# Kernel optimization log

Hardware: AMD Instinct MI355X
Metric: run time of the kernel (lower is better)

## Reference

```python
import jax, jax.numpy as jnp
import numpy as np

B, N, D, H, F = 2, 2048, 1024, 16, 4096
E = D // H
EPS = 1e-5

def layer_norm(x, g, b):
    mu = jnp.mean(x, axis=-1, keepdims=True)
    var = jnp.var(x, axis=-1, keepdims=True)
    return (x - mu) * jax.lax.rsqrt(var + EPS) * g + b

def setup_inputs() -> dict:
    key = jax.random.key(0)
    ks = jax.random.split(key, 16)
    s = lambda k, sh, fan: jax.random.normal(k, sh, jnp.float32) * (1.0 / np.sqrt(fan))
    return {
        'x': jax.random.normal(ks[0], (B, N, D), jnp.float32),
        'wq': s(ks[1], (D, D), D), 'bq': jnp.zeros((D,), jnp.float32),
        'wk': s(ks[2], (D, D), D), 'bk': jnp.zeros((D,), jnp.float32),
        'wv': s(ks[3], (D, D), D), 'bv': jnp.zeros((D,), jnp.float32),
        'w1': s(ks[4], (F, D), D), 'b1': jnp.zeros((F,), jnp.float32),
        'ln_mlp_g': jnp.ones((F,), jnp.float32), 'ln_mlp_b': jnp.zeros((F,), jnp.float32),
        'w2': s(ks[5], (D, F), F), 'b2': jnp.zeros((D,), jnp.float32),
        'ln1_g': jnp.ones((D,), jnp.float32), 'ln1_b': jnp.zeros((D,), jnp.float32),
        'ln2_g': jnp.ones((D,), jnp.float32), 'ln2_b': jnp.zeros((D,), jnp.float32),
    }

def reference(x, wq, bq, wk, bk, wv, bv, w1, b1, ln_mlp_g, ln_mlp_b, w2, b2, ln1_g, ln1_b, ln2_g, ln2_b):
    h = layer_norm(x, ln1_g, ln1_b)                       # [B,N,D]
    q = (h @ wq.T + bq).reshape(B, N, H, E).transpose(0, 2, 1, 3)  # [B,H,N,E]
    k = (h @ wk.T + bk).reshape(B, N, H, E).transpose(0, 2, 1, 3)
    v = (h @ wv.T + bv).reshape(B, N, H, E).transpose(0, 2, 1, 3)
    # faithful to source: score = q@k^T / sqrt(1/emb_dim) == q@k^T * sqrt(emb_dim)
    score = jnp.einsum('bhne,bhme->bhnm', q, k) * np.sqrt(D).astype(np.float32)
    causal = jnp.tril(jnp.ones((N, N), bool))
    score = jnp.where(causal[None, None], score, -jnp.inf)
    weight = jax.nn.softmax(score, axis=-1)
    attn = jnp.einsum('bhnm,bhme->bhne', weight, v)       # [B,H,N,E]
    attn = attn.transpose(0, 2, 1, 3).reshape(B, N, D)
    x = x + attn
    h2 = layer_norm(x, ln2_g, ln2_b)
    m = h2 @ w1.T + b1                                    # [B,N,F]
    m = jax.nn.relu(layer_norm(m, ln_mlp_g, ln_mlp_b))
    # faithful: no second residual in the source forward
    return m @ w2.T + b2
```

## Files before the change

### kernel.cpp

```cpp
#include <hip/hip_runtime.h>
#include <cstdint>

typedef __bf16 bf16_t;
typedef bf16_t bf16x8 __attribute__((ext_vector_type(8)));
typedef bf16_t bf16x4 __attribute__((ext_vector_type(4)));
typedef float  floatx4 __attribute__((ext_vector_type(4)));

#define GLD_LDS(g, l) __builtin_amdgcn_global_load_lds( \
    (const __attribute__((address_space(1))) unsigned int*)(g), \
    (__attribute__((address_space(3))) unsigned int*)(l), 16, 0, 0)

#define MFMA_BF16_16x16x32 __builtin_amdgcn_mfma_f32_16x16x32_bf16

__global__ __launch_bounds__(256) void prep(
    const float* __restrict__ wq, const float* __restrict__ wk,
    const float* __restrict__ wv, const float* __restrict__ w1,
    const float* __restrict__ w2, const float* __restrict__ bq,
    const float* __restrict__ bk,
    bf16_t* __restrict__ wqk_hi, bf16_t* __restrict__ wqk_lo,
    bf16_t* __restrict__ wvb, bf16_t* __restrict__ w1b, bf16_t* __restrict__ w2b,
    float* __restrict__ bqk) {
  const int blk = blockIdx.x, tid = threadIdx.x;
  if (blk < 2048) {
    const int qk = blk >> 10;
    const int i  = (blk & 1023) * 256 + tid;
    const float* src = qk ? wk : wq;
    float4 v = ((const float4*)src)[i];
    float f[4] = {v.x, v.y, v.z, v.w};
    bf16x4 h, l;
    #pragma unroll
    for (int j = 0; j < 4; ++j) { h[j] = (bf16_t)f[j]; l[j] = (bf16_t)(f[j] - (float)h[j]); }
    ((bf16x4*)(wqk_hi + qk * 1024 * 1024))[i] = h;
    ((bf16x4*)(wqk_lo + qk * 1024 * 1024))[i] = l;
  } else if (blk < 3072) {
    const int i = (blk - 2048) * 256 + tid;
    float4 v = ((const float4*)wv)[i];
    bf16x4 o; o[0]=(bf16_t)v.x; o[1]=(bf16_t)v.y; o[2]=(bf16_t)v.z; o[3]=(bf16_t)v.w;
    ((bf16x4*)wvb)[i] = o;
  } else if (blk < 7168) {
    const int i = (blk - 3072) * 256 + tid;
    float4 v = ((const float4*)w1)[i];
    bf16x4 o; o[0]=(bf16_t)v.x; o[1]=(bf16_t)v.y; o[2]=(bf16_t)v.z; o[3]=(bf16_t)v.w;
    ((bf16x4*)w1b)[i] = o;
  } else if (blk < 11264) {
    const int i = (blk - 7168) * 256 + tid;
    float4 v = ((const float4*)w2)[i];
    bf16x4 o; o[0]=(bf16_t)v.x; o[1]=(bf16_t)v.y; o[2]=(bf16_t)v.z; o[3]=(bf16_t)v.w;
    ((bf16x4*)w2b)[i] = o;
  } else {
    const int i = (blk - 11264) * 256 + tid;
    if (i < 1024) { bqk[i] = bq[i]; bqk[1024 + i] = bk[i]; }
  }
}


__device__ __forceinline__ void block_sum2(float& s, float& ss, float* red) {
  #pragma unroll
  for (int off = 32; off > 0; off >>= 1) {
    s  += __shfl_down(s, off);
    ss += __shfl_down(ss, off);
  }
  const int wave = threadIdx.x >> 6;
  if ((threadIdx.x & 63) == 0) { red[wave * 2] = s; red[wave * 2 + 1] = ss; }
  __syncthreads();
  s  = red[0] + red[2] + red[4] + red[6];
  ss = red[1] + red[3] + red[5] + red[7];
}

__global__ __launch_bounds__(256) void ln_fwd_split(const float* __restrict__ x,
    const float* __restrict__ g, const float* __restrict__ b,
    bf16_t* __restrict__ out_hi, bf16_t* __restrict__ out_lo) {
  __shared__ float red[8];
  const size_t row = blockIdx.x;
  float4 v = ((const float4*)(x + row * 1024))[threadIdx.x];
  float s  = v.x + v.y + v.z + v.w;
  float ss = v.x*v.x + v.y*v.y + v.z*v.z + v.w*v.w;
  block_sum2(s, ss, red);
  const float mu  = s * (1.f / 1024.f);
  const float var = ss * (1.f / 1024.f) - mu * mu;
  const float rs  = rsqrtf(var + 1e-5f);
  float4 gg = ((const float4*)g)[threadIdx.x];
  float4 bb = ((const float4*)b)[threadIdx.x];
  float f[4];
  f[0] = (v.x - mu) * rs * gg.x + bb.x;
  f[1] = (v.y - mu) * rs * gg.y + bb.y;
  f[2] = (v.z - mu) * rs * gg.z + bb.z;
  f[3] = (v.w - mu) * rs * gg.w + bb.w;
  bf16x4 oh, ol;
  #pragma unroll
  for (int j = 0; j < 4; ++j) {
    oh[j] = (bf16_t)f[j];
    ol[j] = (bf16_t)(f[j] - (float)oh[j]);
  }
  ((bf16x4*)(out_hi + row * 1024))[threadIdx.x] = oh;
  ((bf16x4*)(out_lo + row * 1024))[threadIdx.x] = ol;
}

__global__ __launch_bounds__(256) void resid_ln_fwd(const float* __restrict__ x,
    const float* __restrict__ a, const float* __restrict__ g, const float* __restrict__ b,
    bf16_t* __restrict__ out) {
  __shared__ float red[8];
  const size_t row = blockIdx.x;
  float4 v = ((const float4*)(x + row * 1024))[threadIdx.x];
  float4 av = ((const float4*)(a + row * 1024))[threadIdx.x];
  v.x += av.x; v.y += av.y; v.z += av.z; v.w += av.w;
  float s  = v.x + v.y + v.z + v.w;
  float ss = v.x*v.x + v.y*v.y + v.z*v.z + v.w*v.w;
  block_sum2(s, ss, red);
  const float mu  = s * (1.f / 1024.f);
  const float var = ss * (1.f / 1024.f) - mu * mu;
  const float rs  = rsqrtf(var + 1e-5f);
  float4 gg = ((const float4*)g)[threadIdx.x];
  float4 bb = ((const float4*)b)[threadIdx.x];
  bf16x4 o;
  o[0] = (bf16_t)((v.x - mu) * rs * gg.x + bb.x);
  o[1] = (bf16_t)((v.y - mu) * rs * gg.y + bb.y);
  o[2] = (bf16_t)((v.z - mu) * rs * gg.z + bb.z);
  o[3] = (bf16_t)((v.w - mu) * rs * gg.w + bb.w);
  ((bf16x4*)(out + row * 1024))[threadIdx.x] = o;
}

__global__ __launch_bounds__(256) void ln_relu_inplace(bf16_t* __restrict__ m,
    const float* __restrict__ g, const float* __restrict__ b) {
  __shared__ float red[8];
  const size_t row = blockIdx.x;
  bf16_t* mr = m + row * 4096;
  const int base = threadIdx.x * 16;
  bf16x8 v0 = *(bf16x8*)(mr + base);
  bf16x8 v1 = *(bf16x8*)(mr + base + 8);
  float f[16];
  #pragma unroll
  for (int i = 0; i < 8; ++i) { f[i] = (float)v0[i]; f[8 + i] = (float)v1[i]; }
  float s = 0.f, ss = 0.f;
  #pragma unroll
  for (int i = 0; i < 16; ++i) { s += f[i]; ss += f[i] * f[i]; }
  block_sum2(s, ss, red);
  const float mu  = s * (1.f / 4096.f);
  const float var = ss * (1.f / 4096.f) - mu * mu;
  const float rs  = rsqrtf(var + 1e-5f);
  bf16x8 o0, o1;
  #pragma unroll
  for (int i = 0; i < 16; ++i) {
    float ov = (f[i] - mu) * rs * g[base + i] + b[base + i];
    ov = fmaxf(ov, 0.f);
    if (i < 8) o0[i] = (bf16_t)ov; else o1[i - 8] = (bf16_t)ov;
  }
  *(bf16x8*)(mr + base) = o0;
  *(bf16x8*)(mr + base + 8) = o1;
}

template <int OUT_MODE, int BM>
__global__ __launch_bounds__(256) void gemm_bt(
    const bf16_t* __restrict__ A, const bf16_t* __restrict__ Bw,
    const float* __restrict__ bias, void* __restrict__ Cp,
    int M, int N, int K) {
  constexpr int MI = BM / 32;
  __shared__ bf16_t As[BM * 32];
  __shared__ bf16_t Bs[128 * 32];
  const int tid  = threadIdx.x;
  const int wave = tid >> 6, lane = tid & 63;
  const int quad = lane >> 4, l15 = lane & 15;
  const int m0 = blockIdx.x * BM, n0 = blockIdx.y * 128;
  const int wm = (wave >> 1) * (BM / 2), wn = (wave & 1) * 64;
  const int srowA = wave * (BM / 4) + (lane >> 2);
  const int srowB = wave * 32 + (lane >> 2);
  const int scol = (lane & 3) * 8;

  floatx4 acc[MI][4] = {};

  const bf16_t* Ag = A  + (size_t)(m0 + srowA) * K + scol;
  const bf16_t* Bg = Bw + (size_t)(n0 + srowB) * K + scol;

  for (int k0 = 0; k0 < K; k0 += 32) {
    __syncthreads();
    #pragma unroll
    for (int i = 0; i < BM / 64; ++i)
      GLD_LDS(Ag + (size_t)(i * 16) * K + k0, As + wave * (BM / 4) * 32 + i * 512);
    #pragma unroll
    for (int i = 0; i < 2; ++i)
      GLD_LDS(Bg + (size_t)(i * 16) * K + k0, Bs + wave * 1024 + i * 512);
    __syncthreads();
    bf16x8 af[MI], bfr[4];
    #pragma unroll
    for (int i = 0; i < MI; ++i)
      af[i] = *(const bf16x8*)(As + (wm + i * 16 + l15) * 32 + quad * 8);
    #pragma unroll
    for (int j = 0; j < 4; ++j)
      bfr[j] = *(const bf16x8*)(Bs + (wn + j * 16 + l15) * 32 + quad * 8);
    #pragma unroll
    for (int i = 0; i < MI; ++i)
      #pragma unroll
      for (int j = 0; j < 4; ++j)
        acc[i][j] = MFMA_BF16_16x16x32(af[i], bfr[j], acc[i][j], 0, 0, 0);
  }
  #pragma unroll
  for (int j = 0; j < 4; ++j) {
    const int col = n0 + wn + j * 16 + l15;
    const float bv = bias[col];
    #pragma unroll
    for (int i = 0; i < MI; ++i) {
      #pragma unroll
      for (int r = 0; r < 4; ++r) {
        const int row = m0 + wm + i * 16 + quad * 4 + r;
        const float v = acc[i][j][r] + bv;
        if (OUT_MODE == 0) {
          ((float*)Cp)[(size_t)row * N + col] = v;
        } else if (OUT_MODE == 1) {
          ((bf16_t*)Cp)[(size_t)row * N + col] = (bf16_t)v;
        } else {
          const int b = row >> 11, n = row & 2047;
          const int h = col >> 6, e = col & 63;
          ((bf16_t*)Cp)[(((size_t)((b << 4) + h) * 2048 + n) << 6) + e] = (bf16_t)v;
        }
      }
    }
  }
}

__global__ __launch_bounds__(256) void gemm_qk_split(
    const bf16_t* __restrict__ Ah, const bf16_t* __restrict__ Al,
    const bf16_t* __restrict__ Bh, const bf16_t* __restrict__ Bl,
    const float* __restrict__ bias,
    bf16_t* __restrict__ qhi, bf16_t* __restrict__ qlo,
    bf16_t* __restrict__ khi, bf16_t* __restrict__ klo,
    int M, int N, int K) {
  __shared__ bf16_t Ash[64 * 32];
  __shared__ bf16_t Asl[64 * 32];
  __shared__ bf16_t Bsh[128 * 32];
  __shared__ bf16_t Bsl[128 * 32];
  const int tid  = threadIdx.x;
  const int wave = tid >> 6, lane = tid & 63;
  const int quad = lane >> 4, l15 = lane & 15;
  const int m0 = blockIdx.x * 64, n0 = blockIdx.y * 128;
  const int wm = (wave >> 1) * 32, wn = (wave & 1) * 64;
  const int srowA = wave * 16 + (lane >> 2);
  const int srowB = wave * 32 + (lane >> 2);
  const int scol = (lane & 3) * 8;

  floatx4 acc[2][4] = {};

  const size_t aoff = (size_t)(m0 + srowA) * K + scol;
  const size_t boff = (size_t)(n0 + srowB) * K + scol;

  for (int k0 = 0; k0 < K; k0 += 32) {
    __syncthreads();
    GLD_LDS(Ah + aoff + k0, Ash + wave * 512);
    GLD_LDS(Al + aoff + k0, Asl + wave * 512);
    #pragma unroll
    for (int i = 0; i < 2; ++i) {
      const size_t gb = boff + (size_t)(i * 16) * K + k0;
      GLD_LDS(Bh + gb, Bsh + wave * 1024 + i * 512);
      GLD_LDS(Bl + gb, Bsl + wave * 1024 + i * 512);
    }
    __syncthreads();
    bf16x8 ah[2], al[2], bh[4], bl[4];
    #pragma unroll
    for (int i = 0; i < 2; ++i) {
      const int ro = (wm + i * 16 + l15) * 32 + quad * 8;
      ah[i] = *(const bf16x8*)(Ash + ro);
      al[i] = *(const bf16x8*)(Asl + ro);
    }
    #pragma unroll
    for (int j = 0; j < 4; ++j) {
      const int ro = (wn + j * 16 + l15) * 32 + quad * 8;
      bh[j] = *(const bf16x8*)(Bsh + ro);
      bl[j] = *(const bf16x8*)(Bsl + ro);
    }
    #pragma unroll
    for (int i = 0; i < 2; ++i)
      #pragma unroll
      for (int j = 0; j < 4; ++j) {
        acc[i][j] = MFMA_BF16_16x16x32(ah[i], bh[j], acc[i][j], 0, 0, 0);
        acc[i][j] = MFMA_BF16_16x16x32(ah[i], bl[j], acc[i][j], 0, 0, 0);
        acc[i][j] = MFMA_BF16_16x16x32(al[i], bh[j], acc[i][j], 0, 0, 0);
      }
  }
  #pragma unroll
  for (int j = 0; j < 4; ++j) {
    const int col = n0 + wn + j * 16 + l15;
    const float bv = bias[col];
    const bool isq = col < 1024;
    bf16_t* hib = isq ? qhi : khi;
    bf16_t* lob = isq ? qlo : klo;
    const float scale = isq ? 32.0f : 1.0f;
    const int h = (col >> 6) & 15, e = col & 63;
    #pragma unroll
    for (int i = 0; i < 2; ++i) {
      #pragma unroll
      for (int r = 0; r < 4; ++r) {
        const int row = m0 + wm + i * 16 + quad * 4 + r;
        const int b = row >> 11, n = row & 2047;
        const float c = (acc[i][j][r] + bv) * scale;
        const bf16_t chi = (bf16_t)c;
        const bf16_t clo = (bf16_t)(c - (float)chi);
        const size_t dst = (((size_t)((b << 4) + h) * 2048 + n) << 6) + e;
        hib[dst] = chi;
        lob[dst] = clo;
      }
    }
  }
}

__global__ __launch_bounds__(256) void transpose_v(
    const bf16_t* __restrict__ vhm, bf16_t* __restrict__ vT) {
  __shared__ bf16_t T[64 * 72];
  const int bh = blockIdx.x, n0 = blockIdx.y * 64;
  const int r = threadIdx.x >> 2;
  const int c = (threadIdx.x & 3) * 16;
  const bf16_t* src = vhm + ((size_t)bh * 2048 + n0 + r) * 64 + c;
  bf16x8 a0 = *(const bf16x8*)src;
  bf16x8 a1 = *(const bf16x8*)(src + 8);
  #pragma unroll
  for (int j = 0; j < 8; ++j) {
    T[(c + j) * 72 + r]     = a0[j];
    T[(c + 8 + j) * 72 + r] = a1[j];
  }
  __syncthreads();
  bf16x8 o0 = *(const bf16x8*)(T + r * 72 + c);
  bf16x8 o1 = *(const bf16x8*)(T + r * 72 + c + 8);
  bf16_t* dst = vT + ((size_t)(bh * 64 + r)) * 2048 + n0 + c;
  *(bf16x8*)dst = o0;
  *(bf16x8*)(dst + 8) = o1;
}

__global__ __launch_bounds__(256, 4) void attn_causal(
    const bf16_t* __restrict__ qhi, const bf16_t* __restrict__ qlo,
    const bf16_t* __restrict__ khi, const bf16_t* __restrict__ klo,
    const bf16_t* __restrict__ vT, float* __restrict__ o) {
  __shared__ bf16_t KsH[64 * 72];
  __shared__ bf16_t KsL[64 * 72];
  __shared__ bf16_t Vt[64 * 72];
  __shared__ bf16_t Ps[4][16 * 70];

  const int tid  = threadIdx.x;
  const int wave = tid >> 6, lane = tid & 63;
  const int quad = lane >> 4, l15 = lane & 15;
  const int bh = blockIdx.x;
  const int q0 = (31 - (int)blockIdx.y) * 64;
  const size_t hb = (size_t)bh * 2048;

  const int wmin = q0 + wave * 16;
  bf16x8 qh[2], ql[2];
  {
    const bf16_t* qbh = qhi + ((hb + wmin + l15) << 6) + quad * 8;
    const bf16_t* qbl = qlo + ((hb + wmin + l15) << 6) + quad * 8;
    qh[0] = *(const bf16x8*)qbh;
    qh[1] = *(const bf16x8*)(qbh + 32);
    ql[0] = *(const bf16x8*)qbl;
    ql[1] = *(const bf16x8*)(qbl + 32);
  }

  floatx4 accO[4] = {};
  float m_row[4] = {-1e30f, -1e30f, -1e30f, -1e30f};
  float l_row[4] = {};

  const int kr = wave * 16 + (lane >> 3);
  const int kc = (lane & 7) * 8;
  const bf16_t* kgh = khi + ((hb + kr) << 6) + kc;
  const bf16_t* kgl = klo + ((hb + kr) << 6) + kc;
  const bf16_t* vg  = vT + ((size_t)(bh * 64 + kr)) * 2048 + kc;

  bf16x8 pkh0 = *(const bf16x8*)(kgh);
  bf16x8 pkh1 = *(const bf16x8*)(kgh + (8 << 6));
  bf16x8 pkl0 = *(const bf16x8*)(kgl);
  bf16x8 pkl1 = *(const bf16x8*)(kgl + (8 << 6));
  bf16x8 pv0  = *(const bf16x8*)(vg);
  bf16x8 pv1  = *(const bf16x8*)(vg + 8 * 2048);

  const int ntiles = (q0 >> 6) + 1;
  for (int t = 0; t < ntiles; ++t) {
    const int k0 = t * 64;
    __syncthreads();
    *(bf16x8*)(KsH + kr * 72 + kc)       = pkh0;
    *(bf16x8*)(KsH + (kr + 8) * 72 + kc) = pkh1;
    *(bf16x8*)(KsL + kr * 72 + kc)       = pkl0;
    *(bf16x8*)(KsL + (kr + 8) * 72 + kc) = pkl1;
    *(bf16x8*)(Vt  + kr * 72 + kc)       = pv0;
    *(bf16x8*)(Vt  + (kr + 8) * 72 + kc) = pv1;
    if (t + 1 < ntiles) {
      const int koff = (t + 1) << 12;
      pkh0 = *(const bf16x8*)(kgh + koff);
      pkh1 = *(const bf16x8*)(kgh + koff + (8 << 6));
      pkl0 = *(const bf16x8*)(kgl + koff);
      pkl1 = *(const bf16x8*)(kgl + koff + (8 << 6));
      pv0  = *(const bf16x8*)(vg + (t + 1) * 64);
      pv1  = *(const bf16x8*)(vg + (t + 1) * 64 + 8 * 2048);
    }
    __syncthreads();

    const bool needmask = (k0 + 63 > wmin);

    floatx4 sv[4];
    #pragma unroll
    for (int j = 0; j < 4; ++j) {
      const bf16_t* kbh = KsH + (j * 16 + l15) * 72;
      const bf16_t* kbl = KsL + (j * 16 + l15) * 72;
      const bf16x8 kh0 = *(const bf16x8*)(kbh + quad * 8);
      const bf16x8 kh1 = *(const bf16x8*)(kbh + 32 + quad * 8);
      const bf16x8 kl0 = *(const bf16x8*)(kbl + quad * 8);
      const bf16x8 kl1 = *(const bf16x8*)(kbl + 32 + quad * 8);
      floatx4 acc = {};
      acc = MFMA_BF16_16x16x32(qh[0], kh0, acc, 0, 0, 0);
      acc = MFMA_BF16_16x16x32(qh[1], kh1, acc, 0, 0, 0);
      acc = MFMA_BF16_16x16x32(qh[0], kl0, acc, 0, 0, 0);
      acc = MFMA_BF16_16x16x32(qh[1], kl1, acc, 0, 0, 0);
      acc = MFMA_BF16_16x16x32(ql[0], kh0, acc, 0, 0, 0);
      acc = MFMA_BF16_16x16x32(ql[1], kh1, acc, 0, 0, 0);
      sv[j] = acc;
    }

    const int colb = k0 + l15;
    #pragma unroll
    for (int r = 0; r < 4; ++r) {
      const int rowg = wmin + quad * 4 + r;
      float sr[4], mr = -1e30f;
      #pragma unroll
      for (int j = 0; j < 4; ++j) {
        float x = sv[j][r];
        if (needmask && (colb + j * 16 > rowg)) x = -1e30f;
        sr[j] = x;
        mr = fmaxf(mr, x);
      }
      mr = fmaxf(mr, __shfl_xor(mr, 1));
      mr = fmaxf(mr, __shfl_xor(mr, 2));
      mr = fmaxf(mr, __shfl_xor(mr, 4));
      mr = fmaxf(mr, __shfl_xor(mr, 8));
      const float mnew = fmaxf(m_row[r], mr);
      const float alpha = __expf(m_row[r] - mnew);
      m_row[r] = mnew;
      float psum = 0.f;
      #pragma unroll
      for (int j = 0; j < 4; ++j) {
        const float p = __expf(sr[j] - mnew);
        const bf16_t pb = (bf16_t)p;
        psum += (float)pb;
        Ps[wave][(quad * 4 + r) * 70 + j * 16 + l15] = pb;
      }
      psum += __shfl_xor(psum, 1);
      psum += __shfl_xor(psum, 2);
      psum += __shfl_xor(psum, 4);
      psum += __shfl_xor(psum, 8);
      l_row[r] = l_row[r] * alpha + psum;
      #pragma unroll
      for (int j = 0; j < 4; ++j) accO[j][r] *= alpha;
    }
    asm volatile("s_waitcnt lgkmcnt(0)" ::: "memory");

    bf16x8 pf[2];
    {
      const bf16_t* pr = &Ps[wave][l15 * 70];
      pf[0] = *(const bf16x8*)(pr + quad * 8);
      pf[1] = *(const bf16x8*)(pr + 32 + quad * 8);
    }
    #pragma unroll
    for (int j = 0; j < 4; ++j) {
      const bf16_t* vb = Vt + (j * 16 + l15) * 72;
      const bf16x8 vf0 = *(const bf16x8*)(vb + quad * 8);
      const bf16x8 vf1 = *(const bf16x8*)(vb + 32 + quad * 8);
      accO[j] = MFMA_BF16_16x16x32(pf[0], vf0, accO[j], 0, 0, 0);
      accO[j] = MFMA_BF16_16x16x32(pf[1], vf1, accO[j], 0, 0, 0);
    }
  }

  const int b = bh >> 4, h = bh & 15;
  #pragma unroll
  for (int r = 0; r < 4; ++r) {
    const float linv = 1.f / l_row[r];
    const int qr = wmin + quad * 4 + r;
    float* orow = o + ((size_t)(b * 2048) + qr) * 1024 + h * 64;
    #pragma unroll
    for (int j = 0; j < 4; ++j)
      orow[j * 16 + l15] = accO[j][r] * linv;
  }
}


extern "C" void kernel_launch(void* const* d_in, const int* in_sizes, int n_in,
                              void* d_out, int out_size, void* d_ws, size_t ws_size,
                              hipStream_t stream) {
  const float* x        = (const float*)d_in[0];
  const float* wq       = (const float*)d_in[1];
  const float* bq       = (const float*)d_in[2];
  const float* wk       = (const float*)d_in[3];
  const float* bk       = (const float*)d_in[4];
  const float* wv       = (const float*)d_in[5];
  const float* bv       = (const float*)d_in[6];
  const float* w1       = (const float*)d_in[7];
  const float* b1       = (const float*)d_in[8];
  const float* ln_mlp_g = (const float*)d_in[9];
  const float* ln_mlp_b = (const float*)d_in[10];
  const float* w2       = (const float*)d_in[11];
  const float* b2       = (const float*)d_in[12];
  const float* ln1_g    = (const float*)d_in[13];
  const float* ln1_b    = (const float*)d_in[14];
  const float* ln2_g    = (const float*)d_in[15];
  const float* ln2_b    = (const float*)d_in[16];

  char* ws = (char*)d_ws;
  bf16_t* h_hi   = (bf16_t*)(ws);
  bf16_t* h_lo   = (bf16_t*)(ws + (8u  << 20));
  bf16_t* vTb    = (bf16_t*)(ws);
  bf16_t* wqk_hi = (bf16_t*)(ws + (16u << 20));
  bf16_t* wqk_lo = (bf16_t*)(ws + (20u << 20));
  bf16_t* wvb    = (bf16_t*)(ws + (24u << 20));
  float*  bqk    = (float*) (ws + (26u << 20));
  bf16_t* w1b    = (bf16_t*)(ws + (28u << 20));
  bf16_t* w2b    = (bf16_t*)(ws + (36u << 20));
  bf16_t* qhi    = (bf16_t*)(ws + (44u << 20));
  bf16_t* qlo    = (bf16_t*)(ws + (52u << 20));
  bf16_t* khi    = (bf16_t*)(ws + (60u << 20));
  bf16_t* klo    = (bf16_t*)(ws + (68u << 20));
  bf16_t* mbuf   = (bf16_t*)(ws + (44u << 20));
  bf16_t* vhm    = (bf16_t*)(ws + (76u << 20));
  float*  attnb  = (float*) (ws + (84u << 20));
  bf16_t* h2     = (bf16_t*)(ws + (100u << 20));

  prep<<<11268, 256, 0, stream>>>(wq, wk, wv, w1, w2, bq, bk,
                                  wqk_hi, wqk_lo, wvb, w1b, w2b, bqk);

  ln_fwd_split<<<4096, 256, 0, stream>>>(x, ln1_g, ln1_b, h_hi, h_lo);
  gemm_qk_split<<<dim3(64, 16), 256, 0, stream>>>(h_hi, h_lo, wqk_hi, wqk_lo, bqk,
                                                  qhi, qlo, khi, klo, 4096, 2048, 1024);
  gemm_bt<2, 64><<<dim3(64, 8), 256, 0, stream>>>(h_hi, wvb, bv, vhm, 4096, 1024, 1024);
  transpose_v<<<dim3(32, 32), 256, 0, stream>>>(vhm, vTb);
  attn_causal<<<dim3(32, 32), 256, 0, stream>>>(qhi, qlo, khi, klo, vTb, attnb);
  resid_ln_fwd<<<4096, 256, 0, stream>>>(x, attnb, ln2_g, ln2_b, h2);
  gemm_bt<1, 128><<<dim3(32, 32), 256, 0, stream>>>(h2, w1b, b1, mbuf, 4096, 4096, 1024);
  ln_relu_inplace<<<4096, 256, 0, stream>>>(mbuf, ln_mlp_g, ln_mlp_b);
  gemm_bt<0, 64><<<dim3(64, 8), 256, 0, stream>>>(mbuf, w2b, b2, d_out, 4096, 1024, 4096);

  (void)in_sizes; (void)n_in; (void)out_size; (void)ws_size;
}
```

Baseline: 478.0 us.

## Transpose QK^T MFMA so each lane owns one query row in softmax

Swaps the MFMA operand order so the score tile comes out transposed, giving each lane a single query row across 16 key columns. Row max and sum then need only two cross-lane shuffles instead of four per row times four rows, and the running m/l statistics shrink to one scalar per lane. P is written to LDS as bf16x4 vectors rather than scalar stores. The accumulator rescale is skipped when no row max changed in the wave. In exchange it adds shuffles to broadcast alpha and l back to the output layout.

After: 472.8 us. Within noise of the previous version (-1.1%).

```diff
diff --git a/kernel.cpp b/kernel.cpp
--- a/kernel.cpp
+++ b/kernel.cpp
@@ -340,6 +340,7 @@
   const size_t hb = (size_t)bh * 2048;
 
   const int wmin = q0 + wave * 16;
+  const int qrow = wmin + l15;
   bf16x8 qh[2], ql[2];
   {
     const bf16_t* qbh = qhi + ((hb + wmin + l15) << 6) + quad * 8;
@@ -351,8 +352,8 @@
   }
 
   floatx4 accO[4] = {};
-  float m_row[4] = {-1e30f, -1e30f, -1e30f, -1e30f};
-  float l_row[4] = {};
+  float m_row = -1e30f;
+  float l_row = 0.f;
 
   const int kr = wave * 16 + (lane >> 3);
   const int kc = (lane & 7) * 8;
@@ -400,49 +401,59 @@
       const bf16x8 kl0 = *(const bf16x8*)(kbl + quad * 8);
       const bf16x8 kl1 = *(const bf16x8*)(kbl + 32 + quad * 8);
       floatx4 acc = {};
-      acc = MFMA_BF16_16x16x32(qh[0], kh0, acc, 0, 0, 0);
-      acc = MFMA_BF16_16x16x32(qh[1], kh1, acc, 0, 0, 0);
-      acc = MFMA_BF16_16x16x32(qh[0], kl0, acc, 0, 0, 0);
-      acc = MFMA_BF16_16x16x32(qh[1], kl1, acc, 0, 0, 0);
-      acc = MFMA_BF16_16x16x32(ql[0], kh0, acc, 0, 0, 0);
-      acc = MFMA_BF16_16x16x32(ql[1], kh1, acc, 0, 0, 0);
+      acc = MFMA_BF16_16x16x32(kh0, qh[0], acc, 0, 0, 0);
+      acc = MFMA_BF16_16x16x32(kh1, qh[1], acc, 0, 0, 0);
+      acc = MFMA_BF16_16x16x32(kl0, qh[0], acc, 0, 0, 0);
+      acc = MFMA_BF16_16x16x32(kl1, qh[1], acc, 0, 0, 0);
+      acc = MFMA_BF16_16x16x32(kh0, ql[0], acc, 0, 0, 0);
+      acc = MFMA_BF16_16x16x32(kh1, ql[1], acc, 0, 0, 0);
       sv[j] = acc;
     }
 
-    const int colb = k0 + l15;
-    #pragma unroll
-    for (int r = 0; r < 4; ++r) {
-      const int rowg = wmin + quad * 4 + r;
-      float sr[4], mr = -1e30f;
-      #pragma unroll
-      for (int j = 0; j < 4; ++j) {
+    const int lim = qrow - k0 - quad * 4;
+    float mr = -1e30f;
+    #pragma unroll
+    for (int j = 0; j < 4; ++j)
+      #pragma unroll
+      for (int r = 0; r < 4; ++r) {
         float x = sv[j][r];
-        if (needmask && (colb + j * 16 > rowg)) x = -1e30f;
-        sr[j] = x;
+        if (needmask && (j * 16 + r > lim)) x = -1e30f;
+        sv[j][r] = x;
         mr = fmaxf(mr, x);
       }
-      mr = fmaxf(mr, __shfl_xor(mr, 1));
-      mr = fmaxf(mr, __shfl_xor(mr, 2));
-      mr = fmaxf(mr, __shfl_xor(mr, 4));
-      mr = fmaxf(mr, __shfl_xor(mr, 8));
-      const float mnew = fmaxf(m_row[r], mr);
-      const float alpha = __expf(m_row[r] - mnew);
-      m_row[r] = mnew;
-      float psum = 0.f;
-      #pragma unroll
-      for (int j = 0; j < 4; ++j) {
-        const float p = __expf(sr[j] - mnew);
-        const bf16_t pb = (bf16_t)p;
-        psum += (float)pb;
-        Ps[wave][(quad * 4 + r) * 70 + j * 16 + l15] = pb;
+    mr = fmaxf(mr, __shfl_xor(mr, 16));
+    mr = fmaxf(mr, __shfl_xor(mr, 32));
+    const float mold = m_row;
+    const float mnew = fmaxf(mold, mr);
+    m_row = mnew;
+    float psum = 0.f;
+    bf16x4 pb[4];
+    #pragma unroll
+    for (int j = 0; j < 4; ++j)
+      #pragma unroll
+      for (int r = 0; r < 4; ++r) {
+        const float p = __expf(sv[j][r] - mnew);
+        const bf16_t pv = (bf16_t)p;
+        psum += (float)pv;
+        pb[j][r] = pv;
       }
-      psum += __shfl_xor(psum, 1);
-      psum += __shfl_xor(psum, 2);
-      psum += __shfl_xor(psum, 4);
-      psum += __shfl_xor(psum, 8);
-      l_row[r] = l_row[r] * alpha + psum;
-      #pragma unroll
-      for (int j = 0; j < 4; ++j) accO[j][r] *= alpha;
+    {
+      bf16_t* pw = &Ps[wave][l15 * 70];
+      #pragma unroll
+      for (int j = 0; j < 4; ++j)
+        *(bf16x4*)(pw + j * 16 + quad * 4) = pb[j];
+    }
+    psum += __shfl_xor(psum, 16);
+    psum += __shfl_xor(psum, 32);
+    const float alpha = __expf(mold - mnew);
+    l_row = l_row * alpha + psum;
+    if (__any(mnew > mold)) {
+      #pragma unroll
+      for (int r = 0; r < 4; ++r) {
+        const float ar = __shfl(alpha, quad * 4 + r);
+        #pragma unroll
+        for (int j = 0; j < 4; ++j) accO[j][r] *= ar;
+      }
     }
     asm volatile("s_waitcnt lgkmcnt(0)" ::: "memory");
 
@@ -465,7 +476,8 @@
   const int b = bh >> 4, h = bh & 15;
   #pragma unroll
   for (int r = 0; r < 4; ++r) {
-    const float linv = 1.f / l_row[r];
+    const float lr = __shfl(l_row, quad * 4 + r);
+    const float linv = 1.f / lr;
     const int qr = wmin + quad * 4 + r;
     float* orow = o + ((size_t)(b * 2048) + qr) * 1024 + h * 64;
     #pragma unroll
```
